# Kernel optimization log

Hardware: AMD Instinct MI355X
Metric: run time of the kernel (lower is better)

## Reference

```python
import jax, jax.numpy as jnp
import numpy as np
from jax import lax

KERNEL = 2  # kernel_size, forced by the (s3-1, s4-1, s5-1) output reshape


def setup_inputs() -> dict:
    key = jax.random.key(0)
    kx, kw = jax.random.split(key)
    x = jax.random.normal(kx, (4, 16, 32, 32, 32), dtype=jnp.float32)
    w = jax.random.normal(kw, (512, 128), dtype=jnp.float32)  # (d1, d2=C*2^3)
    return {"x": x, "w": w}


def _gaussian_kernel(x, w):
    N, C, D, H, W = x.shape
    d1, d2 = w.shape
    # 3D unfold with kernel 2, stride 1, no padding -> (N, C*8, D-1, H-1, W-1)
    patches = lax.conv_general_dilated_patches(
        x,
        filter_shape=(KERNEL, KERNEL, KERNEL),
        window_strides=(1, 1, 1),
        padding='VALID',
    )
    P = (D - 1) * (H - 1) * (W - 1)
    y = patches.reshape(N, d2, P).transpose(0, 2, 1)  # (N, P, d2)
    # sum((y - w)^2) expanded as ||y||^2 - 2 y.w + ||w||^2 to avoid the
    # (N, P, d1, d2) broadcasted difference tensor.
    y_sq = jnp.sum(y * y, axis=-1, keepdims=True)           # (N, P, 1)
    w_sq = jnp.sum(w * w, axis=-1)                          # (d1,)
    cross = jnp.einsum('npd,kd->npk', y, w)                 # (N, P, d1)
    dist = y_sq - 2.0 * cross + w_sq                        # (N, P, d1)
    out = jnp.exp(-dist)
    return out.transpose(0, 2, 1).reshape(N, d1, D - 1, H - 1, W - 1)


def reference(x, w):
    return _gaussian_kernel(x, w)
```

## Files before the change

### kernel.cpp

```cpp
#include <hip/hip_runtime.h>

typedef unsigned char u8;
typedef float f32x4 __attribute__((ext_vector_type(4)));
typedef float f4u __attribute__((ext_vector_type(4), aligned(4)));

#define P_OUT 29791
#define NCH   512

__device__ __forceinline__ unsigned pk4_fp8(float a, float b, float c, float d) {
  int v = __builtin_amdgcn_cvt_pk_fp8_f32(a, b, 0, false);
  v = __builtin_amdgcn_cvt_pk_fp8_f32(c, d, v, true);
  return (unsigned)v;
}

__global__ void wprep_kernel(const float* __restrict__ w,
                             u8* __restrict__ wb, float* __restrict__ wsq) {
  const int tid = threadIdx.x;
  const int g = blockIdx.x * 16 + (tid >> 4);
  const int c = tid & 15;
  const float4* wr = (const float4*)(w + g * 128 + c * 8);
  float4 f0 = wr[0], f1 = wr[1];
  float s = f0.x*f0.x + f0.y*f0.y + f0.z*f0.z + f0.w*f0.w
          + f1.x*f1.x + f1.y*f1.y + f1.z*f1.z + f1.w*f1.w;
#pragma unroll
  for (int m = 1; m < 16; m <<= 1) s += __shfl_xor(s, m, 64);
  uint2 pk;
  pk.x = pk4_fp8(f0.x, f0.y, f0.z, f0.w);
  pk.y = pk4_fp8(f1.x, f1.y, f1.z, f1.w);
  *(uint2*)(wb + g * 128 + c * 8) = pk;
  if (c == 0) wsq[g] = s;
}

#define GLDS(g, l) __builtin_amdgcn_global_load_lds(                         \
    (const __attribute__((address_space(1))) unsigned int*)(g),              \
    (__attribute__((address_space(3))) unsigned int*)(l), 16, 0, 0)

#define LGKM_BAR() do {                                                      \
    asm volatile("s_waitcnt lgkmcnt(0)\n\ts_barrier" ::: "memory");          \
    __builtin_amdgcn_sched_barrier(0);                                       \
  } while (0)

__global__ __launch_bounds__(256, 2)
void gauss_fused_kernel(const float* __restrict__ x,
                        const u8* __restrict__ wb,
                        const float* __restrict__ wsq,
                        float* __restrict__ out) {
  __shared__ __align__(16) u8 SMEM[37888];
  u8* Ws = SMEM;
  float* Xs = (float*)(SMEM + 16384);
  float* Ep = (float*)SMEM;

  const int bid = blockIdx.x;
  const int tile = (bid & 7) * 496 + (bid >> 3);
  const unsigned nb = (unsigned)tile / 992u;
  const unsigned rem = (unsigned)tile - nb * 992u;
  const unsigned ct = rem / 248u;
  const unsigned r2 = rem - ct * 248u;
  const unsigned d  = r2 >> 3;
  const unsigned hb = r2 & 7;
  const int h0 = hb * 4;
  const int nh = (h0 + 4 <= 31) ? 4 : (31 - h0);
  const int nrows = nh * 31;
  const int c0 = ct * 128;
  const int tp0 = d * 961 + h0 * 31;

  const int tid = threadIdx.x;
  const int wid = tid >> 6;
  const int lane = tid & 63;
  const int quad = lane >> 4;
  const int col = lane & 15;
  const int wch = wid & 1;
  const int wp = wid >> 1;

#pragma unroll
  for (int t = 0; t < 4; ++t) {
    const int Lb = (wid * 4 + t) * 64;
    const int L = Lb + lane;
    const int row = L >> 3;
    const int jc = (L & 7) ^ (row & 7);
    GLDS(wb + (size_t)(c0 + row) * 128 + jc * 16, &Ws[Lb * 16]);
  }

#pragma unroll
  for (int t = 0; t < 6; ++t) {
    if (t < 5 || wid == 0) {
      const int Lb = t * 256 + wid * 64;
      const int L = Lb + lane;
      unsigned c = (unsigned)L / 82u;
      if (c > 15u) c = 15u;
      unsigned rc = (unsigned)L - c * 82u;
      if (rc > 79u) rc = 79u;
      const unsigned kd = rc / 40u;
      const unsigned rr = rc - kd * 40u;
      const unsigned hq = rr >> 3;
      const int jc = (int)(rr & 7u);
      const int hg = h0 + (int)hq;
      const int hcl = (hg < 31) ? hg : 31;
      GLDS(x + (((size_t)(nb * 16 + c)) << 15) + (d + kd) * 1024 + hcl * 32 + jc * 4,
           &Xs[Lb * 4]);
    }
  }

  int rb[4];
  int xoff[4];
#pragma unroll
  for (int j = 0; j < 4; ++j) {
    rb[j] = wp * 64 + j * 16 + col;
    const unsigned rc = (unsigned)((rb[j] < nrows) ? rb[j] : (nrows - 1));
    const unsigned hh = rc / 31u;
    const unsigned wv = rc - hh * 31u;
    xoff[j] = (int)(hh * 32 + wv);
  }

  f32x4 acc[4][4];
#pragma unroll
  for (int i = 0; i < 4; ++i)
#pragma unroll
    for (int j = 0; j < 4; ++j) acc[i][j] = (f32x4){0.f, 0.f, 0.f, 0.f};

  float sq[4] = {0.f, 0.f, 0.f, 0.f};

  __syncthreads();

  const int c16b = quad >> 1;
  const int hoff = (quad & 1) * 8;
#pragma unroll
  for (int ks = 0; ks < 4; ++ks) {
    long long a[4], b[4];
#pragma unroll
    for (int i = 0; i < 4; ++i) {
      const int rowA = wch * 64 + i * 16 + col;
      const int pa = (ks * 2 + c16b) ^ (rowA & 7);
      a[i] = *(const long long*)&Ws[rowA * 128 + pa * 16 + hoff];
    }
    const int cc = ks * 4 + quad;
    const float* xb = &Xs[cc * 328];
#pragma unroll
    for (int j = 0; j < 4; ++j) {
      const float* pB = xb + xoff[j];
      const float v0 = pB[0],   v1 = pB[1],   v2 = pB[32],  v3 = pB[33];
      const float v4 = pB[160], v5 = pB[161], v6 = pB[192], v7 = pB[193];
      sq[j] += v0*v0 + v1*v1 + v2*v2 + v3*v3 + v4*v4 + v5*v5 + v6*v6 + v7*v7;
      const unsigned lo = pk4_fp8(v0, v1, v2, v3);
      const unsigned hi = pk4_fp8(v4, v5, v6, v7);
      b[j] = (long long)(((unsigned long long)hi << 32) | lo);
    }
#pragma unroll
    for (int i = 0; i < 4; ++i)
#pragma unroll
      for (int j = 0; j < 4; ++j)
        acc[i][j] = __builtin_amdgcn_mfma_f32_16x16x32_fp8_fp8(a[i], b[j],
                                                               acc[i][j], 0, 0, 0);
  }
#pragma unroll
  for (int j = 0; j < 4; ++j) {
    sq[j] += __shfl_xor(sq[j], 16, 64);
    sq[j] += __shfl_xor(sq[j], 32, 64);
  }

  LGKM_BAR();

  const int hw = lane >> 5;
  const int ll = lane & 31;
  const int nfull = (nrows == 124) ? 31 : 23;
#pragma unroll
  for (int pa = 0; pa < 2; ++pa) {
#pragma unroll
    for (int ii = 0; ii < 2; ++ii) {
      const int i = pa * 2 + ii;
#pragma unroll
      for (int r = 0; r < 4; ++r) {
        const int ch2 = wch * 32 + ii * 16 + quad * 4 + r;
        const int chl = wch * 64 + pa * 32 + ii * 16 + quad * 4 + r;
        const float wsv = wsq[c0 + chl];
#pragma unroll
        for (int j = 0; j < 4; ++j)
          Ep[ch2 * 132 + rb[j]] = __expf(2.f * acc[i][j][r] - sq[j] - wsv);
      }
    }
    LGKM_BAR();

#pragma unroll
    for (int rr = 0; rr < 8; ++rr) {
      const int ch2 = wid * 16 + rr * 2 + hw;
      const int chl = (ch2 >> 5) * 64 + pa * 32 + (ch2 & 31);
      float* ob = out + ((size_t)(nb * NCH + c0 + chl)) * P_OUT + tp0;
      if (ll < nfull) {
        const f4u v = *(const f4u*)&Ep[ch2 * 132 + 4 * ll];
        *(f4u*)(ob + 4 * ll) = v;
      } else if (ll == 23 && nrows == 93) {
        ob[92] = Ep[ch2 * 132 + 92];
      }
    }
    if (pa == 0) LGKM_BAR();
  }
}

extern "C" void kernel_launch(void* const* d_in, const int* in_sizes, int n_in,
                              void* d_out, int out_size, void* d_ws, size_t ws_size,
                              hipStream_t stream) {
  const float* x = (const float*)d_in[0];
  const float* w = (const float*)d_in[1];
  float* out = (float*)d_out;
  char* ws = (char*)d_ws;
  u8* wb     = (u8*)ws;
  float* wsq = (float*)(ws + 65536);

  wprep_kernel<<<32, 256, 0, stream>>>(w, wb, wsq);
  gauss_fused_kernel<<<3968, 256, 0, stream>>>(x, wb, wsq, out);
}
```

Baseline: 253.4 us.

## Loop over all channel tiles per block, reusing packed x fragments with double-buffered weights

Each block now handles all 512 output channels for its spatial tile instead of one 128-channel slice. The x patch fragments are converted to fp8 and their squared norms computed once, kept in registers, and reused for four weight tiles. The weight tiles are double-buffered in LDS with async global-to-LDS loads overlapped with the exp/store epilogue. This cuts the grid to a quarter of its blocks and removes redundant x loads and conversions, at the cost of more LDS per block (which may reduce occupancy) and a longer serial chain of work per block.

```diff
diff --git a/kernel.cpp b/kernel.cpp
--- a/kernel.cpp
+++ b/kernel.cpp
@@ -40,28 +40,31 @@
     __builtin_amdgcn_sched_barrier(0);                                       \
   } while (0)
 
+#define VMC_BAR() do {                                                       \
+    asm volatile("s_waitcnt vmcnt(16)\n\ts_barrier" ::: "memory");           \
+    __builtin_amdgcn_sched_barrier(0);                                       \
+  } while (0)
+
 __global__ __launch_bounds__(256, 2)
 void gauss_fused_kernel(const float* __restrict__ x,
                         const u8* __restrict__ wb,
                         const float* __restrict__ wsq,
                         float* __restrict__ out) {
-  __shared__ __align__(16) u8 SMEM[37888];
-  u8* Ws = SMEM;
-  float* Xs = (float*)(SMEM + 16384);
-  float* Ep = (float*)SMEM;
+  __shared__ __align__(16) u8 SMEM[66560];
+  u8* Ws0 = SMEM;
+  u8* Ws1 = SMEM + 16384;
+  float* Xs = (float*)(SMEM + 32768);
+  float* Ep = (float*)(SMEM + 32768);
 
   const int bid = blockIdx.x;
-  const int tile = (bid & 7) * 496 + (bid >> 3);
-  const unsigned nb = (unsigned)tile / 992u;
-  const unsigned rem = (unsigned)tile - nb * 992u;
-  const unsigned ct = rem / 248u;
-  const unsigned r2 = rem - ct * 248u;
+  const int tile = (bid & 7) * 124 + (bid >> 3);
+  const unsigned nb = (unsigned)tile / 248u;
+  const unsigned r2 = (unsigned)tile - nb * 248u;
   const unsigned d  = r2 >> 3;
   const unsigned hb = r2 & 7;
   const int h0 = hb * 4;
   const int nh = (h0 + 4 <= 31) ? 4 : (31 - h0);
   const int nrows = nh * 31;
-  const int c0 = ct * 128;
   const int tp0 = d * 961 + h0 * 31;
 
   const int tid = threadIdx.x;
@@ -78,7 +81,7 @@
     const int L = Lb + lane;
     const int row = L >> 3;
     const int jc = (L & 7) ^ (row & 7);
-    GLDS(wb + (size_t)(c0 + row) * 128 + jc * 16, &Ws[Lb * 16]);
+    GLDS(wb + (size_t)row * 128 + jc * 16, &Ws0[Lb * 16]);
   }
 
 #pragma unroll
@@ -112,27 +115,21 @@
     xoff[j] = (int)(hh * 32 + wv);
   }
 
-  f32x4 acc[4][4];
-#pragma unroll
-  for (int i = 0; i < 4; ++i)
-#pragma unroll
-    for (int j = 0; j < 4; ++j) acc[i][j] = (f32x4){0.f, 0.f, 0.f, 0.f};
-
+  __syncthreads();
+
+#pragma unroll
+  for (int t = 0; t < 4; ++t) {
+    const int Lb = (wid * 4 + t) * 64;
+    const int L = Lb + lane;
+    const int row = L >> 3;
+    const int jc = (L & 7) ^ (row & 7);
+    GLDS(wb + (size_t)(128 + row) * 128 + jc * 16, &Ws1[Lb * 16]);
+  }
+
+  long long B[4][4];
   float sq[4] = {0.f, 0.f, 0.f, 0.f};
-
-  __syncthreads();
-
-  const int c16b = quad >> 1;
-  const int hoff = (quad & 1) * 8;
 #pragma unroll
   for (int ks = 0; ks < 4; ++ks) {
-    long long a[4], b[4];
-#pragma unroll
-    for (int i = 0; i < 4; ++i) {
-      const int rowA = wch * 64 + i * 16 + col;
-      const int pa = (ks * 2 + c16b) ^ (rowA & 7);
-      a[i] = *(const long long*)&Ws[rowA * 128 + pa * 16 + hoff];
-    }
     const int cc = ks * 4 + quad;
     const float* xb = &Xs[cc * 328];
 #pragma unroll
@@ -143,14 +140,8 @@
       sq[j] += v0*v0 + v1*v1 + v2*v2 + v3*v3 + v4*v4 + v5*v5 + v6*v6 + v7*v7;
       const unsigned lo = pk4_fp8(v0, v1, v2, v3);
       const unsigned hi = pk4_fp8(v4, v5, v6, v7);
-      b[j] = (long long)(((unsigned long long)hi << 32) | lo);
-    }
-#pragma unroll
-    for (int i = 0; i < 4; ++i)
-#pragma unroll
-      for (int j = 0; j < 4; ++j)
-        acc[i][j] = __builtin_amdgcn_mfma_f32_16x16x32_fp8_fp8(a[i], b[j],
-                                                               acc[i][j], 0, 0, 0);
+      B[ks][j] = (long long)(((unsigned long long)hi << 32) | lo);
+    }
   }
 #pragma unroll
   for (int j = 0; j < 4; ++j) {
@@ -158,41 +149,87 @@
     sq[j] += __shfl_xor(sq[j], 32, 64);
   }
 
-  LGKM_BAR();
-
+  const int c16b = quad >> 1;
+  const int hoff = (quad & 1) * 8;
   const int hw = lane >> 5;
   const int ll = lane & 31;
   const int nfull = (nrows == 124) ? 31 : 23;
-#pragma unroll
-  for (int pa = 0; pa < 2; ++pa) {
-#pragma unroll
-    for (int ii = 0; ii < 2; ++ii) {
-      const int i = pa * 2 + ii;
-#pragma unroll
-      for (int r = 0; r < 4; ++r) {
-        const int ch2 = wch * 32 + ii * 16 + quad * 4 + r;
-        const int chl = wch * 64 + pa * 32 + ii * 16 + quad * 4 + r;
-        const float wsv = wsq[c0 + chl];
+
+#pragma unroll
+  for (int ct = 0; ct < 4; ++ct) {
+    if (ct > 0) VMC_BAR();
+    const u8* Wcur = (ct & 1) ? Ws1 : Ws0;
+
+    f32x4 acc[4][4];
+#pragma unroll
+    for (int i = 0; i < 4; ++i)
+#pragma unroll
+      for (int j = 0; j < 4; ++j) acc[i][j] = (f32x4){0.f, 0.f, 0.f, 0.f};
+
+#pragma unroll
+    for (int ks = 0; ks < 4; ++ks) {
+      long long a[4];
+#pragma unroll
+      for (int i = 0; i < 4; ++i) {
+        const int rowA = wch * 64 + i * 16 + col;
+        const int pa = (ks * 2 + c16b) ^ (rowA & 7);
+        a[i] = *(const long long*)&Wcur[rowA * 128 + pa * 16 + hoff];
+      }
+#pragma unroll
+      for (int i = 0; i < 4; ++i)
 #pragma unroll
         for (int j = 0; j < 4; ++j)
-          Ep[ch2 * 132 + rb[j]] = __expf(2.f * acc[i][j][r] - sq[j] - wsv);
-      }
-    }
+          acc[i][j] = __builtin_amdgcn_mfma_f32_16x16x32_fp8_fp8(a[i], B[ks][j],
+                                                                 acc[i][j], 0, 0, 0);
+    }
+
     LGKM_BAR();
 
-#pragma unroll
-    for (int rr = 0; rr < 8; ++rr) {
-      const int ch2 = wid * 16 + rr * 2 + hw;
-      const int chl = (ch2 >> 5) * 64 + pa * 32 + (ch2 & 31);
-      float* ob = out + ((size_t)(nb * NCH + c0 + chl)) * P_OUT + tp0;
-      if (ll < nfull) {
-        const f4u v = *(const f4u*)&Ep[ch2 * 132 + 4 * ll];
-        *(f4u*)(ob + 4 * ll) = v;
-      } else if (ll == 23 && nrows == 93) {
-        ob[92] = Ep[ch2 * 132 + 92];
-      }
-    }
-    if (pa == 0) LGKM_BAR();
+    if (ct < 2) {
+      u8* Wn = (ct & 1) ? Ws1 : Ws0;
+      const int cb = (ct + 2) * 128;
+#pragma unroll
+      for (int t = 0; t < 4; ++t) {
+        const int Lb = (wid * 4 + t) * 64;
+        const int L = Lb + lane;
+        const int row = L >> 3;
+        const int jc = (L & 7) ^ (row & 7);
+        GLDS(wb + (size_t)(cb + row) * 128 + jc * 16, &Wn[Lb * 16]);
+      }
+    }
+
+    const int c0 = ct * 128;
+#pragma unroll
+    for (int pa = 0; pa < 2; ++pa) {
+#pragma unroll
+      for (int ii = 0; ii < 2; ++ii) {
+        const int i = pa * 2 + ii;
+#pragma unroll
+        for (int r = 0; r < 4; ++r) {
+          const int ch2 = wch * 32 + ii * 16 + quad * 4 + r;
+          const int chl = wch * 64 + pa * 32 + ii * 16 + quad * 4 + r;
+          const float wsv = wsq[c0 + chl];
+#pragma unroll
+          for (int j = 0; j < 4; ++j)
+            Ep[ch2 * 132 + rb[j]] = __expf(2.f * acc[i][j][r] - sq[j] - wsv);
+        }
+      }
+      LGKM_BAR();
+
+#pragma unroll
+      for (int rr = 0; rr < 8; ++rr) {
+        const int ch2 = wid * 16 + rr * 2 + hw;
+        const int chl = (ch2 >> 5) * 64 + pa * 32 + (ch2 & 31);
+        float* ob = out + ((size_t)(nb * NCH + c0 + chl)) * P_OUT + tp0;
+        if (ll < nfull) {
+          const f4u v = *(const f4u*)&Ep[ch2 * 132 + 4 * ll];
+          *(f4u*)(ob + 4 * ll) = v;
+        } else if (ll == 23 && nrows == 93) {
+          ob[92] = Ep[ch2 * 132 + 92];
+        }
+      }
+      if (pa == 0) LGKM_BAR();
+    }
   }
 }
 
@@ -207,5 +244,5 @@
   float* wsq = (float*)(ws + 65536);
 
   wprep_kernel<<<32, 256, 0, stream>>>(w, wb, wsq);
-  gauss_fused_kernel<<<3968, 256, 0, stream>>>(x, wb, wsq, out);
-}
+  gauss_fused_kernel<<<992, 256, 0, stream>>>(x, wb, wsq, out);
+}
```

Result: no change. 251.6 us, median of 2 (-0.7%).
